# Performance work log

Measured on AMD Instinct MI355X. Metric: run time of the kernel, lower is better.

Reference implementation:

```python
import jax, jax.numpy as jnp
import numpy as np
from jax import lax

H_HID, W_HID = 8, 12
N_PAIR = H_HID * W_HID   # 96
NF = 32                  # mlp_nfilters
C_FEAT = 512 + 2         # phi_im channels + (x,y) coords


def _conv_relu(x, w, b):
    # 3x3 conv, stride 1, SAME padding (SingleConvBlock), then ReLU
    y = lax.conv_general_dilated(x, w, (1, 1), 'SAME',
                                 dimension_numbers=('NCHW', 'OIHW', 'NCHW'))
    return jax.nn.relu(y + b[None, :, None, None])


def _maxpool2(x):
    return lax.reduce_window(x, -jnp.inf, lax.max, (1, 1, 2, 2), (1, 1, 2, 2), 'VALID')


def setup_inputs() -> dict:
    key = jax.random.key(0)
    ks = jax.random.split(key, 16)
    d = {}
    d['x'] = jax.random.normal(ks[0], (4, 3, 64, 96), jnp.float32)
    d['sen_embed'] = jax.random.normal(ks[1], (4, 384), jnp.float32)

    def p(k, shape, fan_in):
        return (jax.random.normal(k, shape, jnp.float32) / np.float32(np.sqrt(fan_in)))

    d['enc1_w'] = p(ks[2], (64, 3, 3, 3), 3 * 9);      d['enc1_b'] = p(ks[3], (64,), 64)
    d['enc2_w'] = p(ks[4], (128, 64, 3, 3), 64 * 9);   d['enc2_b'] = p(ks[5], (128,), 128)
    d['enc3_w'] = p(ks[6], (256, 128, 3, 3), 128 * 9); d['enc3_b'] = p(ks[7], (256,), 256)
    d['enc4_w'] = p(ks[8], (512, 256, 3, 3), 256 * 9); d['enc4_b'] = p(ks[9], (512,), 512)
    d['g1_w'] = p(ks[10], (1412, 256), 1412);          d['g1_b'] = p(ks[11], (256,), 256)
    d['g2_w'] = p(ks[12], (256, 256), 256);            d['g2_b'] = p(ks[13], (256,), 256)
    d['g3_w'] = p(ks[14], (256, N_PAIR * NF), 256);    d['g3_b'] = p(ks[15], (N_PAIR * NF,), N_PAIR * NF)
    return d


def _forward(x, sen_embed, enc1_w, enc1_b, enc2_w, enc2_b, enc3_w, enc3_b,
             enc4_w, enc4_b, g1_w, g1_b, g2_w, g2_b, g3_w, g3_b):
    # ---- conv encoder ----
    e1 = _conv_relu(x, enc1_w, enc1_b)                     # [B,64,64,96]
    e2 = _conv_relu(_maxpool2(e1), enc2_w, enc2_b)         # [B,128,32,48]
    e3 = _conv_relu(_maxpool2(e2), enc3_w, enc3_b)         # [B,256,16,24]
    phi_im = _conv_relu(_maxpool2(e3), enc4_w, enc4_b)     # [B,512,8,12]
    B = phi_im.shape[0]

    # ---- coordinate grid (matches torch.meshgrid default 'ij' then reshape) ----
    xc = jnp.linspace(-1.0, 1.0, W_HID, dtype=phi_im.dtype)
    yc = jnp.linspace(-1.0, 1.0, H_HID, dtype=phi_im.dtype)
    xg, yg = jnp.meshgrid(xc, yc, indexing='ij')           # each [12,8]
    coord = jnp.stack([xg.reshape(H_HID, W_HID), yg.reshape(H_HID, W_HID)], axis=0)
    coord = jnp.broadcast_to(coord[None], (B, 2, H_HID, W_HID))

    # per-location features F: [B, n_pair, 514]
    F = jnp.concatenate([phi_im, coord], axis=1).reshape(B, C_FEAT, N_PAIR).transpose(0, 2, 1)

    # ---- all-pairs relation network ----
    # pair feature at (a,c) = concat(F[c], F[a], sen_embed); exploit linearity of first
    # Linear to avoid materializing the [B,n,n,1412] concat tensor (same math).
    A, Bm, Cm = g1_w[:C_FEAT], g1_w[C_FEAT:2 * C_FEAT], g1_w[2 * C_FEAT:]
    u = F @ A                                # i-part,  [B,n,256]
    v = F @ Bm                               # j-part,  [B,n,256]
    ws = sen_embed @ Cm + g1_b               # sentence part, [B,256]
    h1 = jax.nn.relu(u[:, None, :, :] + v[:, :, None, :] + ws[:, None, None, :])  # [B,n,n,256]
    h2 = jax.nn.relu(h1 @ g2_w + g2_b)                                           # [B,n,n,256]
    out = jax.nn.relu(h2 @ g3_w + g3_b)                                          # [B,n,n,3072]

    # sum over all n_pair^2 pairs, reshape to feature map [B,32,8,12]
    phi = out.sum(axis=(1, 2)).reshape(B, NF, H_HID, W_HID)
    return phi


def reference(x, sen_embed, enc1_w, enc1_b, enc2_w, enc2_b, enc3_w, enc3_b,
              enc4_w, enc4_b, g1_w, g1_b, g2_w, g2_b, g3_w, g3_b):
    return _forward(x, sen_embed, enc1_w, enc1_b, enc2_w, enc2_b, enc3_w, enc3_b,
                    enc4_w, enc4_b, g1_w, g1_b, g2_w, g2_b, g3_w, g3_b)
```

## Files before the change

kernel.cpp:

```cpp
#include <hip/hip_runtime.h>
#include <hip/hip_bf16.h>

using bf16 = __hip_bfloat16;
typedef __attribute__((ext_vector_type(8))) short short8;
typedef __attribute__((ext_vector_type(4))) float f32x4;

static __device__ __forceinline__ bf16 f2b(float x) { return __float2bfloat16(x); }
static __device__ __forceinline__ float b2f(bf16 x) { return __bfloat162float(x); }
static __device__ __forceinline__ short fb(float x) {
  bf16 h = __float2bfloat16(fmaxf(x, 0.f));
  return *(short*)&h;
}

static __device__ __forceinline__ void gload_lds16(const void* g, void* l) {
  auto gp = (const __attribute__((address_space(1))) unsigned int*)g;
  auto lp = (__attribute__((address_space(3))) unsigned int*)l;
  __builtin_amdgcn_global_load_lds(gp, lp, 16, 0, 0);
}

__global__ void conv1pool_kernel(const float* __restrict__ x, const float* __restrict__ w,
                                 const float* __restrict__ bias, bf16* __restrict__ out) {
  const int H = 64, W = 96, HW = H * W;
  __shared__ float wl[27 * 64];
  int tid = threadIdx.x;
  for (int idx = tid; idx < 27 * 64; idx += 256) {
    int k = idx >> 6, oc_ = idx & 63;
    wl[idx] = w[oc_ * 27 + k];
  }
  __syncthreads();
  int oc = tid & 63;
  int pp = blockIdx.x * 4 + (tid >> 6);
  int b = pp / 1536, rem = pp - b * 1536;
  int yp = rem / 48, xp = rem - yp * 48;
  int y0 = 2 * yp - 1, x0 = 2 * xp - 1;
  float win[3][4][4];
  #pragma unroll
  for (int ic = 0; ic < 3; ++ic) {
    const float* xsrc = x + ((size_t)b * 3 + ic) * HW;
    #pragma unroll
    for (int dy = 0; dy < 4; ++dy) {
      int yy = y0 + dy;
      #pragma unroll
      for (int dx = 0; dx < 4; ++dx) {
        int xx = x0 + dx;
        win[ic][dy][dx] = (yy >= 0 && yy < H && xx >= 0 && xx < W) ? xsrc[yy * W + xx] : 0.f;
      }
    }
  }
  float cmax = -1e30f;
  #pragma unroll
  for (int sy = 0; sy < 2; ++sy)
    #pragma unroll
    for (int sx = 0; sx < 2; ++sx) {
      float acc = 0.f;
      #pragma unroll
      for (int ic = 0; ic < 3; ++ic)
        #pragma unroll
        for (int ky = 0; ky < 3; ++ky)
          #pragma unroll
          for (int kx = 0; kx < 3; ++kx)
            acc += win[ic][sy + ky][sx + kx] * wl[(ic * 9 + ky * 3 + kx) * 64 + oc];
      cmax = fmaxf(cmax, acc);
    }
  out[(size_t)pp * 64 + oc] = f2b(fmaxf(cmax + bias[oc], 0.f));
}

__global__ void prep_kernel(const float* __restrict__ w2, const float* __restrict__ w3,
                            const float* __restrict__ w4, const float* __restrict__ g1w,
                            const float* __restrict__ sen, float* __restrict__ outz,
                            bf16* __restrict__ w2r, bf16* __restrict__ w3r,
                            bf16* __restrict__ w4r, bf16* __restrict__ wuv,
                            bf16* __restrict__ Fe, float* __restrict__ zb) {
  const int S1 = 73728, S2 = S1 + 294912, S3 = S2 + 1179648, S4 = S3 + 442368,
            S5 = S4 + 12288, S6 = S5 + 24576, S7 = S6 + 36864, S8 = S7 + 64;
  int i = blockIdx.x * 256 + threadIdx.x;
  if (i < S1) {
    int j = i, K = 576, IC = 64;
    int oc = j / K, r = j - oc * K, tap = r / IC, ic = r - tap * IC;
    w2r[j] = f2b(w2[((size_t)oc * IC + ic) * 9 + tap]);
  } else if (i < S2) {
    int j = i - S1, K = 1152, IC = 128;
    int oc = j / K, r = j - oc * K, tap = r / IC, ic = r - tap * IC;
    w3r[j] = f2b(w3[((size_t)oc * IC + ic) * 9 + tap]);
  } else if (i < S3) {
    int j = i - S2, K = 2304, IC = 256;
    int oc = j / K, r = j - oc * K, tap = r / IC, ic = r - tap * IC;
    w4r[j] = f2b(w4[((size_t)oc * IC + ic) * 9 + tap]);
  } else if (i < S4) {
    int j = i - S3;
    int n = j / 576, c = j - n * 576;
    float val = 0.f;
    if (n < 256)      { if (c < 514) val = g1w[(size_t)c * 256 + n]; }
    else if (n < 512) { if (c < 514) val = g1w[(size_t)(514 + c) * 256 + (n - 256)]; }
    else              { if (c < 384) val = g1w[(size_t)(1028 + c) * 256 + (n - 512)]; }
    wuv[j] = f2b(val);
  } else if (i < S5) {
    outz[i - S4] = 0.f;
  } else if (i < S6) {
    int j = i - S5;
    int r = j >> 6, cc = j & 63;
    int p = r % 96;
    float val = 0.f;
    if (cc == 0) val = -1.0f + 2.0f * (float)(p / 8) / 11.0f;
    else if (cc == 1) val = -1.0f + 2.0f * (float)(p % 8) / 7.0f;
    Fe[(size_t)r * 576 + 512 + cc] = f2b(val);
  } else if (i < S7) {
    int j = i - S6;
    int r = j / 576, c = j - r * 576;
    float val = (r < 4 && c < 384) ? sen[r * 384 + c] : 0.f;
    Fe[(size_t)(384 + r) * 576 + c] = f2b(val);
  } else if (i < S8) {
    zb[i - S7] = 0.f;
  }
}

__global__ void transpose2_kernel(const float* __restrict__ g2w, const float* __restrict__ g3w,
                                  bf16* __restrict__ w2t, bf16* __restrict__ w3t) {
  __shared__ bf16 t[32][33];
  int bid = blockIdx.x;
  const float* in;
  bf16* out;
  int R, C, c0, r0;
  if (bid < 64) { in = g2w; out = w2t; R = 256; C = 256; c0 = (bid & 7) * 32; r0 = (bid >> 3) * 32; }
  else { int b2 = bid - 64; in = g3w; out = w3t; R = 256; C = 3072; c0 = (b2 % 96) * 32; r0 = (b2 / 96) * 32; }
  int x = threadIdx.x & 31, y = threadIdx.x >> 5;
  for (int yy = y; yy < 32; yy += 8) {
    int r = r0 + yy, c = c0 + x;
    if (r < R && c < C) t[yy][x] = f2b(in[(size_t)r * C + c]);
  }
  __syncthreads();
  for (int yy = y; yy < 32; yy += 8) {
    int c = c0 + yy, r = r0 + x;
    if (r < R && c < C) out[(size_t)c * R + r] = t[x][yy];
  }
}

template <int CBITS, bool POOL>
__launch_bounds__(256)
__global__ void gemm_conv_kernel(const bf16* __restrict__ pin, const bf16* __restrict__ Wt,
                                 const float* __restrict__ bias, bf16* __restrict__ outb,
                                 const bf16* __restrict__ zbuf,
                                 int Hi, int Wi, int N, int ldout) {
  const int C = 1 << CBITS;
  const int K = 9 << CBITS;
  int m0 = blockIdx.y * 64, n0 = blockIdx.x * 64;
  __shared__ __align__(16) short A_lds[64 * 64];
  __shared__ __align__(16) short B_lds[64 * 64];
  int tid = threadIdx.x, w = tid >> 6, l = tid & 63;
  int quad = l >> 4, l16 = l & 15;
  f32x4 acc[4];
  #pragma unroll
  for (int nt = 0; nt < 4; ++nt)
    #pragma unroll
    for (int e = 0; e < 4; ++e) acc[nt][e] = 0.f;

  int lrow = l >> 3;
  int c_sw = (l & 7) ^ lrow;
  int ybase[2], xbase[2], bidx[2];
  #pragma unroll
  for (int i = 0; i < 2; ++i) {
    int row = m0 + w * 16 + i * 8 + lrow;
    if (POOL) {
      int pg = row >> 2, sub = row & 3;
      int Wh = Wi >> 1, HW2 = (Hi >> 1) * Wh;
      int b = pg / HW2, rem = pg - b * HW2;
      int py = rem / Wh, px = rem - py * Wh;
      bidx[i] = b; ybase[i] = 2 * py + (sub >> 1); xbase[i] = 2 * px + (sub & 1);
    } else {
      int HW = Hi * Wi;
      int b = row / HW, pix = row - b * HW;
      int yy = pix / Wi;
      bidx[i] = b; ybase[i] = yy; xbase[i] = pix - yy * Wi;
    }
  }
  const bf16* bg = Wt + (size_t)(n0 + w * 16 + lrow) * K + c_sw * 8;
  short* al = A_lds + ((size_t)w * 128 + l) * 8;
  short* bl = B_lds + ((size_t)w * 128 + l) * 8;

  for (int kc = 0; kc < K; kc += 64) {
    if (kc) __syncthreads();
    int colt = kc + c_sw * 8;
    int tap = colt >> CBITS, cc = colt & (C - 1);
    int ty = tap / 3, tx = tap - 3 * ty;
    #pragma unroll
    for (int i = 0; i < 2; ++i) {
      int yy = ybase[i] + ty - 1, xx = xbase[i] + tx - 1;
      const bf16* asrc = (yy >= 0 && yy < Hi && xx >= 0 && xx < Wi)
          ? pin + ((((size_t)(bidx[i] * Hi + yy)) * Wi + xx) << CBITS) + cc
          : zbuf;
      gload_lds16(asrc, al + i * 512);
      gload_lds16(bg + kc + (size_t)i * 8 * K, bl + i * 512);
    }
    __syncthreads();
    #pragma unroll
    for (int ks = 0; ks < 64; ks += 32) {
      int cb = (ks >> 3) + quad;
      int mr = w * 16 + l16;
      short8 af = *(const short8*)&A_lds[mr * 64 + ((cb ^ (mr & 7)) * 8)];
      #pragma unroll
      for (int nt = 0; nt < 4; ++nt) {
        int nr = nt * 16 + l16;
        short8 bf = *(const short8*)&B_lds[nr * 64 + ((cb ^ (nr & 7)) * 8)];
        acc[nt] = __builtin_amdgcn_mfma_f32_16x16x32_bf16(af, bf, acc[nt], 0, 0, 0);
      }
    }
  }
  if (POOL) {
    int pg = (m0 + w * 16 + quad * 4) >> 2;
    #pragma unroll
    for (int nt = 0; nt < 4; ++nt) {
      int gcol = n0 + nt * 16 + l16;
      float bv = bias[gcol];
      float m = fmaxf(fmaxf(acc[nt][0], acc[nt][1]), fmaxf(acc[nt][2], acc[nt][3]));
      outb[(size_t)pg * N + gcol] = f2b(fmaxf(m + bv, 0.f));
    }
  } else {
    #pragma unroll
    for (int nt = 0; nt < 4; ++nt) {
      int gcol = n0 + nt * 16 + l16;
      float bv = bias[gcol];
      #pragma unroll
      for (int r = 0; r < 4; ++r) {
        int grow = m0 + w * 16 + quad * 4 + r;
        outb[(size_t)grow * ldout + gcol] = f2b(fmaxf(acc[nt][r] + bv, 0.f));
      }
    }
  }
}

__launch_bounds__(256)
__global__ void gemm64_kernel(const bf16* __restrict__ A, const bf16* __restrict__ Wt,
                              float* __restrict__ outf, int K, int ldout) {
  int m0 = blockIdx.y * 64, n0 = blockIdx.x * 64;
  __shared__ __align__(16) short A_lds[64 * 64];
  __shared__ __align__(16) short B_lds[64 * 64];
  int tid = threadIdx.x, w = tid >> 6, l = tid & 63;
  int quad = l >> 4, l16 = l & 15;
  f32x4 acc[4];
  #pragma unroll
  for (int nt = 0; nt < 4; ++nt)
    #pragma unroll
    for (int e = 0; e < 4; ++e) acc[nt][e] = 0.f;

  int lrow = l >> 3;
  int c_sw = (l & 7) ^ lrow;
  const bf16* ag = A + (size_t)(m0 + w * 16 + lrow) * K + c_sw * 8;
  const bf16* bg = Wt + (size_t)(n0 + w * 16 + lrow) * K + c_sw * 8;
  short* al = A_lds + ((size_t)w * 128 + l) * 8;
  short* bl = B_lds + ((size_t)w * 128 + l) * 8;

  for (int kc = 0; kc < K; kc += 64) {
    if (kc) __syncthreads();
    #pragma unroll
    for (int i = 0; i < 2; ++i) {
      gload_lds16(ag + kc + (size_t)i * 8 * K, al + i * 512);
      gload_lds16(bg + kc + (size_t)i * 8 * K, bl + i * 512);
    }
    __syncthreads();
    #pragma unroll
    for (int ks = 0; ks < 64; ks += 32) {
      int cb = (ks >> 3) + quad;
      int mr = w * 16 + l16;
      short8 af = *(const short8*)&A_lds[mr * 64 + ((cb ^ (mr & 7)) * 8)];
      #pragma unroll
      for (int nt = 0; nt < 4; ++nt) {
        int nr = nt * 16 + l16;
        short8 bf = *(const short8*)&B_lds[nr * 64 + ((cb ^ (nr & 7)) * 8)];
        acc[nt] = __builtin_amdgcn_mfma_f32_16x16x32_bf16(af, bf, acc[nt], 0, 0, 0);
      }
    }
  }
  #pragma unroll
  for (int nt = 0; nt < 4; ++nt) {
    int gcol = n0 + nt * 16 + l16;
    #pragma unroll
    for (int r = 0; r < 4; ++r) {
      int grow = m0 + w * 16 + quad * 4 + r;
      outf[(size_t)grow * ldout + gcol] = acc[nt][r];
    }
  }
}

__launch_bounds__(256)
__global__ void gemm2_kernel(const float* __restrict__ uvws, const float* __restrict__ g1b,
                             const bf16* __restrict__ w2t, const float* __restrict__ g2b,
                             bf16* __restrict__ h2) {
  int b = blockIdx.z;
  int m0 = blockIdx.y * 128;
  int n0 = blockIdx.x * 128;
  __shared__ __align__(16) short A_lds[128 * 64];
  __shared__ __align__(16) short B_lds[128 * 64];
  __shared__ __align__(16) float wsl[256];
  int tid = threadIdx.x, w = tid >> 6, l = tid & 63;
  int quad = l >> 4, l16 = l & 15;
  int mw = (w >> 1) * 64, nw = (w & 1) * 64;
  f32x4 acc[4][4];
  #pragma unroll
  for (int i = 0; i < 4; ++i)
    #pragma unroll
    for (int j = 0; j < 4; ++j)
      #pragma unroll
      for (int e = 0; e < 4; ++e) acc[i][j][e] = 0.f;

  wsl[tid] = uvws[(size_t)(384 + b) * 768 + 512 + tid] + g1b[tid];

  int lrow = l >> 3;
  int c_sw = (l & 7) ^ lrow;
  const bf16* bg = w2t + (size_t)(n0 + w * 32 + lrow) * 256 + c_sw * 8;
  short* bl = B_lds + ((size_t)w * 256 + l) * 8;

  int row = tid >> 1, ks0 = (tid & 1) * 32;
  int m = m0 + row;
  int i_idx = m / 96, j_idx = m - i_idx * 96;
  const float* up = uvws + (size_t)(b * 96 + j_idx) * 768 + ks0;
  const float* vp = uvws + (size_t)(b * 96 + i_idx) * 768 + 256 + ks0;
  __syncthreads();

  for (int kc = 0; kc < 256; kc += 64) {
    if (kc) __syncthreads();
    #pragma unroll
    for (int i = 0; i < 4; ++i)
      gload_lds16(bg + kc + (size_t)i * 8 * 256, bl + i * 512);
    {
      const float4* u4 = (const float4*)(up + kc);
      const float4* v4 = (const float4*)(vp + kc);
      const float4* w4 = (const float4*)&wsl[kc + ks0];
      #pragma unroll
      for (int ch = 0; ch < 4; ++ch) {
        short8 pack;
        #pragma unroll
        for (int q = 0; q < 2; ++q) {
          float4 uu = u4[ch * 2 + q], vv = v4[ch * 2 + q], ww = w4[ch * 2 + q];
          pack[q * 4 + 0] = fb(uu.x + vv.x + ww.x);
          pack[q * 4 + 1] = fb(uu.y + vv.y + ww.y);
          pack[q * 4 + 2] = fb(uu.z + vv.z + ww.z);
          pack[q * 4 + 3] = fb(uu.w + vv.w + ww.w);
        }
        int lc = (ks0 >> 3) + ch;
        *(short8*)&A_lds[row * 64 + ((lc ^ (row & 7)) * 8)] = pack;
      }
    }
    __syncthreads();
    #pragma unroll
    for (int ks = 0; ks < 64; ks += 32) {
      int cb = (ks >> 3) + quad;
      short8 af[4], bfr[4];
      #pragma unroll
      for (int mt = 0; mt < 4; ++mt) {
        int mr = mw + mt * 16 + l16;
        af[mt] = *(const short8*)&A_lds[mr * 64 + ((cb ^ (mr & 7)) * 8)];
      }
      #pragma unroll
      for (int nt = 0; nt < 4; ++nt) {
        int nr = nw + nt * 16 + l16;
        bfr[nt] = *(const short8*)&B_lds[nr * 64 + ((cb ^ (nr & 7)) * 8)];
      }
      #pragma unroll
      for (int mt = 0; mt < 4; ++mt)
        #pragma unroll
        for (int nt = 0; nt < 4; ++nt)
          acc[mt][nt] = __builtin_amdgcn_mfma_f32_16x16x32_bf16(af[mt], bfr[nt], acc[mt][nt], 0, 0, 0);
    }
  }
  bf16* h2b = h2 + (size_t)b * 9216 * 256;
  #pragma unroll
  for (int nt = 0; nt < 4; ++nt) {
    int gcol = n0 + nw + nt * 16 + l16;
    float bias = g2b[gcol];
    #pragma unroll
    for (int mt = 0; mt < 4; ++mt) {
      #pragma unroll
      for (int r = 0; r < 4; ++r) {
        int grow = m0 + mw + mt * 16 + quad * 4 + r;
        h2b[(size_t)grow * 256 + gcol] = f2b(fmaxf(acc[mt][nt][r] + bias, 0.f));
      }
    }
  }
}

__launch_bounds__(256)
__global__ void gemm3_kernel(const bf16* __restrict__ h2, const bf16* __restrict__ w3t,
                             const float* __restrict__ g3b, float* __restrict__ phi) {
  int g = blockIdx.x;
  int x = g & 7, s = g >> 3;
  int grp = s / 24;
  int nIdx = s - grp * 24;
  int mb = grp * 8 + x;
  int b = mb / 72;
  int m0 = (mb - b * 72) * 128;
  int n0 = nIdx * 128;
  __shared__ __align__(16) short A_lds[128 * 64];
  __shared__ __align__(16) short B_lds[128 * 64];
  int tid = threadIdx.x, w = tid >> 6, l = tid & 63;
  int quad = l >> 4, l16 = l & 15;
  int mw = (w >> 1) * 64, nw = (w & 1) * 64;
  f32x4 acc[4][4];
  #pragma unroll
  for (int i = 0; i < 4; ++i)
    #pragma unroll
    for (int j = 0; j < 4; ++j)
      #pragma unroll
      for (int e = 0; e < 4; ++e) acc[i][j][e] = 0.f;

  const int K = 256;
  int lrow = l >> 3;
  int c_sw = (l & 7) ^ lrow;
  const bf16* ag = h2 + (size_t)(b * 9216 + m0 + w * 32 + lrow) * K + c_sw * 8;
  const bf16* bg = w3t + (size_t)(n0 + w * 32 + lrow) * K + c_sw * 8;
  short* al = A_lds + ((size_t)w * 256 + l) * 8;
  short* bl = B_lds + ((size_t)w * 256 + l) * 8;

  for (int kc = 0; kc < K; kc += 64) {
    if (kc) __syncthreads();
    #pragma unroll
    for (int i = 0; i < 4; ++i) {
      gload_lds16(ag + kc + (size_t)i * 8 * K, al + i * 512);
      gload_lds16(bg + kc + (size_t)i * 8 * K, bl + i * 512);
    }
    __syncthreads();
    #pragma unroll
    for (int ks = 0; ks < 64; ks += 32) {
      int cb = (ks >> 3) + quad;
      short8 af[4], bfr[4];
      #pragma unroll
      for (int mt = 0; mt < 4; ++mt) {
        int mr = mw + mt * 16 + l16;
        af[mt] = *(const short8*)&A_lds[mr * 64 + ((cb ^ (mr & 7)) * 8)];
      }
      #pragma unroll
      for (int nt = 0; nt < 4; ++nt) {
        int nr = nw + nt * 16 + l16;
        bfr[nt] = *(const short8*)&B_lds[nr * 64 + ((cb ^ (nr & 7)) * 8)];
      }
      #pragma unroll
      for (int mt = 0; mt < 4; ++mt)
        #pragma unroll
        for (int nt = 0; nt < 4; ++nt)
          acc[mt][nt] = __builtin_amdgcn_mfma_f32_16x16x32_bf16(af[mt], bfr[nt], acc[mt][nt], 0, 0, 0);
    }
  }
  #pragma unroll
  for (int nt = 0; nt < 4; ++nt) {
    int gcol = n0 + nw + nt * 16 + l16;
    float bias = g3b[gcol];
    float s2 = 0.f;
    #pragma unroll
    for (int mt = 0; mt < 4; ++mt)
      #pragma unroll
      for (int r = 0; r < 4; ++r)
        s2 += fmaxf(acc[mt][nt][r] + bias, 0.f);
    s2 += __shfl_xor(s2, 16, 64);
    s2 += __shfl_xor(s2, 32, 64);
    if (quad == 0) atomicAdd(&phi[b * 3072 + gcol], s2);
  }
}

extern "C" void kernel_launch(void* const* d_in, const int* in_sizes, int n_in,
                              void* d_out, int out_size, void* d_ws, size_t ws_size,
                              hipStream_t stream) {
  const float* x   = (const float*)d_in[0];
  const float* sen = (const float*)d_in[1];
  const float* w1  = (const float*)d_in[2];
  const float* b1  = (const float*)d_in[3];
  const float* w2  = (const float*)d_in[4];
  const float* b2  = (const float*)d_in[5];
  const float* w3  = (const float*)d_in[6];
  const float* b3  = (const float*)d_in[7];
  const float* w4  = (const float*)d_in[8];
  const float* b4  = (const float*)d_in[9];
  const float* g1w = (const float*)d_in[10];
  const float* g1b = (const float*)d_in[11];
  const float* g2w = (const float*)d_in[12];
  const float* g2b = (const float*)d_in[13];
  const float* g3w = (const float*)d_in[14];
  const float* g3b = (const float*)d_in[15];
  float* out = (float*)d_out;

  char* wsp = (char*)d_ws;
  size_t off = 0;
  auto alloc = [&](size_t bytes) {
    char* p = wsp + off;
    off += (bytes + 255) & ~(size_t)255;
    return (void*)p;
  };
  bf16* p1   = (bf16*)alloc((size_t)6144 * 64 * 2);
  bf16* p2   = (bf16*)alloc((size_t)1536 * 128 * 2);
  bf16* p3   = (bf16*)alloc((size_t)384 * 256 * 2);
  bf16* Fe   = (bf16*)alloc((size_t)448 * 576 * 2);
  bf16* wuv  = (bf16*)alloc((size_t)768 * 576 * 2);
  float* uvws = (float*)alloc((size_t)448 * 768 * 4);
  bf16* w2r  = (bf16*)alloc((size_t)128 * 576 * 2);
  bf16* w3r  = (bf16*)alloc((size_t)256 * 1152 * 2);
  bf16* w4r  = (bf16*)alloc((size_t)512 * 2304 * 2);
  bf16* w2t  = (bf16*)alloc((size_t)256 * 256 * 2);
  bf16* w3t  = (bf16*)alloc((size_t)3072 * 256 * 2);
  bf16* h2   = (bf16*)alloc((size_t)4 * 9216 * 256 * 2);
  float* zbuf = (float*)alloc((size_t)256);

  prep_kernel<<<dim3(8065), 256, 0, stream>>>(w2, w3, w4, g1w, sen, out, w2r, w3r, w4r, wuv, Fe, zbuf);
  transpose2_kernel<<<dim3(832), 256, 0, stream>>>(g2w, g3w, w2t, w3t);

  conv1pool_kernel<<<dim3(1536), 256, 0, stream>>>(x, w1, b1, p1);
  gemm_conv_kernel<6, true><<<dim3(2, 96), 256, 0, stream>>>(p1, w2r, b2, p2, (const bf16*)zbuf, 32, 48, 128, 128);
  gemm_conv_kernel<7, true><<<dim3(4, 24), 256, 0, stream>>>(p2, w3r, b3, p3, (const bf16*)zbuf, 16, 24, 256, 256);
  gemm_conv_kernel<8, false><<<dim3(8, 6), 256, 0, stream>>>(p3, w4r, b4, Fe, (const bf16*)zbuf, 8, 12, 512, 576);

  gemm64_kernel<<<dim3(12, 7), 256, 0, stream>>>(Fe, wuv, uvws, 576, 768);
  gemm2_kernel<<<dim3(2, 72, 4), 256, 0, stream>>>(uvws, g1b, w2t, g2b, h2);
  gemm3_kernel<<<dim3(6912), 256, 0, stream>>>(h2, w3t, g3b, out);
}
```

Before: 248.1 us.

## Fuse pair-MLP layers 2 and 3 via LDS-resident h2 and merge prep kernels

Replaces the separate gemm2 and gemm3 kernels with one head kernel. Each block computes a 64-row tile of h2 into shared memory and then loops over all 3072 output columns, reducing into phi with atomics. This removes the global h2 round trip (about 19 MB of bf16) and one launch. It also folds conv1pool, prep and the transpose into a single launch. In exchange each block now does a long serial loop over the N dimension with 64-row tiles and a heavy LDS footprint, which lowers occupancy and reuse of the w3t tiles.

```diff
diff --git a/kernel.cpp b/kernel.cpp
--- a/kernel.cpp
+++ b/kernel.cpp
@@ -18,120 +18,121 @@
   __builtin_amdgcn_global_load_lds(gp, lp, 16, 0, 0);
 }
 
-__global__ void conv1pool_kernel(const float* __restrict__ x, const float* __restrict__ w,
-                                 const float* __restrict__ bias, bf16* __restrict__ out) {
-  const int H = 64, W = 96, HW = H * W;
+__global__ void prep_all_kernel(const float* __restrict__ x, const float* __restrict__ w1,
+                                const float* __restrict__ b1, bf16* __restrict__ p1,
+                                const float* __restrict__ w2, const float* __restrict__ w3,
+                                const float* __restrict__ w4, const float* __restrict__ g1w,
+                                const float* __restrict__ sen, float* __restrict__ outz,
+                                bf16* __restrict__ w2r, bf16* __restrict__ w3r,
+                                bf16* __restrict__ w4r, bf16* __restrict__ wuv,
+                                bf16* __restrict__ Fe, float* __restrict__ zb,
+                                const float* __restrict__ g2w, const float* __restrict__ g3w,
+                                bf16* __restrict__ w2t, bf16* __restrict__ w3t) {
   __shared__ float wl[27 * 64];
+  __shared__ bf16 tt[32][33];
+  int bid = blockIdx.x;
   int tid = threadIdx.x;
-  for (int idx = tid; idx < 27 * 64; idx += 256) {
-    int k = idx >> 6, oc_ = idx & 63;
-    wl[idx] = w[oc_ * 27 + k];
-  }
-  __syncthreads();
-  int oc = tid & 63;
-  int pp = blockIdx.x * 4 + (tid >> 6);
-  int b = pp / 1536, rem = pp - b * 1536;
-  int yp = rem / 48, xp = rem - yp * 48;
-  int y0 = 2 * yp - 1, x0 = 2 * xp - 1;
-  float win[3][4][4];
-  #pragma unroll
-  for (int ic = 0; ic < 3; ++ic) {
-    const float* xsrc = x + ((size_t)b * 3 + ic) * HW;
-    #pragma unroll
-    for (int dy = 0; dy < 4; ++dy) {
-      int yy = y0 + dy;
-      #pragma unroll
-      for (int dx = 0; dx < 4; ++dx) {
-        int xx = x0 + dx;
-        win[ic][dy][dx] = (yy >= 0 && yy < H && xx >= 0 && xx < W) ? xsrc[yy * W + xx] : 0.f;
-      }
-    }
-  }
-  float cmax = -1e30f;
-  #pragma unroll
-  for (int sy = 0; sy < 2; ++sy)
-    #pragma unroll
-    for (int sx = 0; sx < 2; ++sx) {
-      float acc = 0.f;
-      #pragma unroll
-      for (int ic = 0; ic < 3; ++ic)
-        #pragma unroll
-        for (int ky = 0; ky < 3; ++ky)
+  if (bid < 1536) {
+    const int H = 64, W = 96, HW = H * W;
+    for (int idx = tid; idx < 27 * 64; idx += 256) {
+      int k = idx >> 6, oc_ = idx & 63;
+      wl[idx] = w1[oc_ * 27 + k];
+    }
+    __syncthreads();
+    int oc = tid & 63;
+    int pp = bid * 4 + (tid >> 6);
+    int b = pp / 1536, rem = pp - b * 1536;
+    int yp = rem / 48, xp = rem - yp * 48;
+    int y0 = 2 * yp - 1, x0 = 2 * xp - 1;
+    float win[3][4][4];
+    #pragma unroll
+    for (int ic = 0; ic < 3; ++ic) {
+      const float* xsrc = x + ((size_t)b * 3 + ic) * HW;
+      #pragma unroll
+      for (int dy = 0; dy < 4; ++dy) {
+        int yy = y0 + dy;
+        #pragma unroll
+        for (int dx = 0; dx < 4; ++dx) {
+          int xx = x0 + dx;
+          win[ic][dy][dx] = (yy >= 0 && yy < H && xx >= 0 && xx < W) ? xsrc[yy * W + xx] : 0.f;
+        }
+      }
+    }
+    float cmax = -1e30f;
+    #pragma unroll
+    for (int sy = 0; sy < 2; ++sy)
+      #pragma unroll
+      for (int sx = 0; sx < 2; ++sx) {
+        float acc = 0.f;
+        #pragma unroll
+        for (int ic = 0; ic < 3; ++ic)
           #pragma unroll
-          for (int kx = 0; kx < 3; ++kx)
-            acc += win[ic][sy + ky][sx + kx] * wl[(ic * 9 + ky * 3 + kx) * 64 + oc];
-      cmax = fmaxf(cmax, acc);
-    }
-  out[(size_t)pp * 64 + oc] = f2b(fmaxf(cmax + bias[oc], 0.f));
-}
-
-__global__ void prep_kernel(const float* __restrict__ w2, const float* __restrict__ w3,
-                            const float* __restrict__ w4, const float* __restrict__ g1w,
-                            const float* __restrict__ sen, float* __restrict__ outz,
-                            bf16* __restrict__ w2r, bf16* __restrict__ w3r,
-                            bf16* __restrict__ w4r, bf16* __restrict__ wuv,
-                            bf16* __restrict__ Fe, float* __restrict__ zb) {
-  const int S1 = 73728, S2 = S1 + 294912, S3 = S2 + 1179648, S4 = S3 + 442368,
-            S5 = S4 + 12288, S6 = S5 + 24576, S7 = S6 + 36864, S8 = S7 + 64;
-  int i = blockIdx.x * 256 + threadIdx.x;
-  if (i < S1) {
-    int j = i, K = 576, IC = 64;
-    int oc = j / K, r = j - oc * K, tap = r / IC, ic = r - tap * IC;
-    w2r[j] = f2b(w2[((size_t)oc * IC + ic) * 9 + tap]);
-  } else if (i < S2) {
-    int j = i - S1, K = 1152, IC = 128;
-    int oc = j / K, r = j - oc * K, tap = r / IC, ic = r - tap * IC;
-    w3r[j] = f2b(w3[((size_t)oc * IC + ic) * 9 + tap]);
-  } else if (i < S3) {
-    int j = i - S2, K = 2304, IC = 256;
-    int oc = j / K, r = j - oc * K, tap = r / IC, ic = r - tap * IC;
-    w4r[j] = f2b(w4[((size_t)oc * IC + ic) * 9 + tap]);
-  } else if (i < S4) {
-    int j = i - S3;
-    int n = j / 576, c = j - n * 576;
-    float val = 0.f;
-    if (n < 256)      { if (c < 514) val = g1w[(size_t)c * 256 + n]; }
-    else if (n < 512) { if (c < 514) val = g1w[(size_t)(514 + c) * 256 + (n - 256)]; }
-    else              { if (c < 384) val = g1w[(size_t)(1028 + c) * 256 + (n - 512)]; }
-    wuv[j] = f2b(val);
-  } else if (i < S5) {
-    outz[i - S4] = 0.f;
-  } else if (i < S6) {
-    int j = i - S5;
-    int r = j >> 6, cc = j & 63;
-    int p = r % 96;
-    float val = 0.f;
-    if (cc == 0) val = -1.0f + 2.0f * (float)(p / 8) / 11.0f;
-    else if (cc == 1) val = -1.0f + 2.0f * (float)(p % 8) / 7.0f;
-    Fe[(size_t)r * 576 + 512 + cc] = f2b(val);
-  } else if (i < S7) {
-    int j = i - S6;
-    int r = j / 576, c = j - r * 576;
-    float val = (r < 4 && c < 384) ? sen[r * 384 + c] : 0.f;
-    Fe[(size_t)(384 + r) * 576 + c] = f2b(val);
-  } else if (i < S8) {
-    zb[i - S7] = 0.f;
-  }
-}
-
-__global__ void transpose2_kernel(const float* __restrict__ g2w, const float* __restrict__ g3w,
-                                  bf16* __restrict__ w2t, bf16* __restrict__ w3t) {
-  __shared__ bf16 t[32][33];
-  int bid = blockIdx.x;
-  const float* in;
-  bf16* out;
-  int R, C, c0, r0;
-  if (bid < 64) { in = g2w; out = w2t; R = 256; C = 256; c0 = (bid & 7) * 32; r0 = (bid >> 3) * 32; }
-  else { int b2 = bid - 64; in = g3w; out = w3t; R = 256; C = 3072; c0 = (b2 % 96) * 32; r0 = (b2 / 96) * 32; }
-  int x = threadIdx.x & 31, y = threadIdx.x >> 5;
-  for (int yy = y; yy < 32; yy += 8) {
-    int r = r0 + yy, c = c0 + x;
-    if (r < R && c < C) t[yy][x] = f2b(in[(size_t)r * C + c]);
-  }
-  __syncthreads();
-  for (int yy = y; yy < 32; yy += 8) {
-    int c = c0 + yy, r = r0 + x;
-    if (r < R && c < C) out[(size_t)c * R + r] = t[x][yy];
+          for (int ky = 0; ky < 3; ++ky)
+            #pragma unroll
+            for (int kx = 0; kx < 3; ++kx)
+              acc += win[ic][sy + ky][sx + kx] * wl[(ic * 9 + ky * 3 + kx) * 64 + oc];
+        cmax = fmaxf(cmax, acc);
+      }
+    p1[(size_t)pp * 64 + oc] = f2b(fmaxf(cmax + b1[oc], 0.f));
+  } else if (bid < 9601) {
+    const int S1 = 73728, S2 = S1 + 294912, S3 = S2 + 1179648, S4 = S3 + 442368,
+              S5 = S4 + 12288, S6 = S5 + 24576, S7 = S6 + 36864, S8 = S7 + 64;
+    int i = (bid - 1536) * 256 + tid;
+    if (i < S1) {
+      int j = i, K = 576, IC = 64;
+      int oc = j / K, r = j - oc * K, tap = r / IC, ic = r - tap * IC;
+      w2r[j] = f2b(w2[((size_t)oc * IC + ic) * 9 + tap]);
+    } else if (i < S2) {
+      int j = i - S1, K = 1152, IC = 128;
+      int oc = j / K, r = j - oc * K, tap = r / IC, ic = r - tap * IC;
+      w3r[j] = f2b(w3[((size_t)oc * IC + ic) * 9 + tap]);
+    } else if (i < S3) {
+      int j = i - S2, K = 2304, IC = 256;
+      int oc = j / K, r = j - oc * K, tap = r / IC, ic = r - tap * IC;
+      w4r[j] = f2b(w4[((size_t)oc * IC + ic) * 9 + tap]);
+    } else if (i < S4) {
+      int j = i - S3;
+      int n = j / 576, c = j - n * 576;
+      float val = 0.f;
+      if (n < 256)      { if (c < 514) val = g1w[(size_t)c * 256 + n]; }
+      else if (n < 512) { if (c < 514) val = g1w[(size_t)(514 + c) * 256 + (n - 256)]; }
+      else              { if (c < 384) val = g1w[(size_t)(1028 + c) * 256 + (n - 512)]; }
+      wuv[j] = f2b(val);
+    } else if (i < S5) {
+      outz[i - S4] = 0.f;
+    } else if (i < S6) {
+      int j = i - S5;
+      int r = j >> 6, cc = j & 63;
+      int p = r % 96;
+      float val = 0.f;
+      if (cc == 0) val = -1.0f + 2.0f * (float)(p / 8) / 11.0f;
+      else if (cc == 1) val = -1.0f + 2.0f * (float)(p % 8) / 7.0f;
+      Fe[(size_t)r * 576 + 512 + cc] = f2b(val);
+    } else if (i < S7) {
+      int j = i - S6;
+      int r = j / 576, c = j - r * 576;
+      float val = (r < 4 && c < 384) ? sen[r * 384 + c] : 0.f;
+      Fe[(size_t)(384 + r) * 576 + c] = f2b(val);
+    } else if (i < S8) {
+      zb[i - S7] = 0.f;
+    }
+  } else {
+    int b2 = bid - 9601;
+    const float* in;
+    bf16* out;
+    int R = 256, C, c0, r0;
+    if (b2 < 64) { in = g2w; out = w2t; C = 256; c0 = (b2 & 7) * 32; r0 = (b2 >> 3) * 32; }
+    else { b2 -= 64; in = g3w; out = w3t; C = 3072; c0 = (b2 % 96) * 32; r0 = (b2 / 96) * 32; }
+    int xq = tid & 31, yq = tid >> 5;
+    for (int yy = yq; yy < 32; yy += 8) {
+      int r = r0 + yy, c = c0 + xq;
+      if (r < R && c < C) tt[yy][xq] = f2b(in[(size_t)r * C + c]);
+    }
+    __syncthreads();
+    for (int yy = yq; yy < 32; yy += 8) {
+      int c = c0 + yy, r = r0 + xq;
+      if (r < R && c < C) out[(size_t)c * R + r] = tt[xq][yy];
+    }
   }
 }
 
@@ -200,8 +201,8 @@
       #pragma unroll
       for (int nt = 0; nt < 4; ++nt) {
         int nr = nt * 16 + l16;
-        short8 bf = *(const short8*)&B_lds[nr * 64 + ((cb ^ (nr & 7)) * 8)];
-        acc[nt] = __builtin_amdgcn_mfma_f32_16x16x32_bf16(af, bf, acc[nt], 0, 0, 0);
+        short8 bf2 = *(const short8*)&B_lds[nr * 64 + ((cb ^ (nr & 7)) * 8)];
+        acc[nt] = __builtin_amdgcn_mfma_f32_16x16x32_bf16(af, bf2, acc[nt], 0, 0, 0);
       }
     }
   }
@@ -265,8 +266,8 @@
       #pragma unroll
       for (int nt = 0; nt < 4; ++nt) {
         int nr = nt * 16 + l16;
-        short8 bf = *(const short8*)&B_lds[nr * 64 + ((cb ^ (nr & 7)) * 8)];
-        acc[nt] = __builtin_amdgcn_mfma_f32_16x16x32_bf16(af, bf, acc[nt], 0, 0, 0);
+        short8 bf2 = *(const short8*)&B_lds[nr * 64 + ((cb ^ (nr & 7)) * 8)];
+        acc[nt] = __builtin_amdgcn_mfma_f32_16x16x32_bf16(af, bf2, acc[nt], 0, 0, 0);
       }
     }
   }
@@ -282,18 +283,28 @@
 }
 
 __launch_bounds__(256)
-__global__ void gemm2_kernel(const float* __restrict__ uvws, const float* __restrict__ g1b,
-                             const bf16* __restrict__ w2t, const float* __restrict__ g2b,
-                             bf16* __restrict__ h2) {
-  int b = blockIdx.z;
-  int m0 = blockIdx.y * 128;
-  int n0 = blockIdx.x * 128;
-  __shared__ __align__(16) short A_lds[128 * 64];
-  __shared__ __align__(16) short B_lds[128 * 64];
-  __shared__ __align__(16) float wsl[256];
+__global__ void head_kernel(const float* __restrict__ uvws, const float* __restrict__ g1b,
+                            const bf16* __restrict__ w2t, const float* __restrict__ g2b,
+                            const bf16* __restrict__ w3t, const float* __restrict__ g3b,
+                            float* __restrict__ out) {
+  __shared__ __align__(16) short h2l[64 * 256];
+  __shared__ __align__(16) short Breg[10240];
+  __shared__ float g3bl[3072];
+  __shared__ float g2bl[256];
+  __shared__ float wsl[256];
+  int blk = blockIdx.x;
+  int b = blk / 144;
+  int m0g = (blk - b * 144) * 64;
   int tid = threadIdx.x, w = tid >> 6, l = tid & 63;
   int quad = l >> 4, l16 = l & 15;
-  int mw = (w >> 1) * 64, nw = (w & 1) * 64;
+
+  wsl[tid] = uvws[(size_t)(384 + b) * 768 + 512 + tid] + g1b[tid];
+  g2bl[tid] = g2b[tid];
+  #pragma unroll
+  for (int i = 0; i < 12; ++i) g3bl[i * 256 + tid] = g3b[i * 256 + tid];
+
+  short* A2 = Breg;
+  short* B2 = Breg + 2048;
   f32x4 acc[4][4];
   #pragma unroll
   for (int i = 0; i < 4; ++i)
@@ -302,156 +313,128 @@
       #pragma unroll
       for (int e = 0; e < 4; ++e) acc[i][j][e] = 0.f;
 
-  wsl[tid] = uvws[(size_t)(384 + b) * 768 + 512 + tid] + g1b[tid];
-
-  int lrow = l >> 3;
-  int c_sw = (l & 7) ^ lrow;
-  const bf16* bg = w2t + (size_t)(n0 + w * 32 + lrow) * 256 + c_sw * 8;
-  short* bl = B_lds + ((size_t)w * 256 + l) * 8;
-
-  int row = tid >> 1, ks0 = (tid & 1) * 32;
-  int m = m0 + row;
-  int i_idx = m / 96, j_idx = m - i_idx * 96;
-  const float* up = uvws + (size_t)(b * 96 + j_idx) * 768 + ks0;
-  const float* vp = uvws + (size_t)(b * 96 + i_idx) * 768 + 256 + ks0;
+  int arow = tid >> 2, aseg = tid & 3;
+  int mA = m0g + arow;
+  int i_idx = mA / 96, j_idx = mA - i_idx * 96;
+  const float* up = uvws + (size_t)(b * 96 + j_idx) * 768;
+  const float* vp = uvws + (size_t)(b * 96 + i_idx) * 768 + 256;
+  int brow = w * 64 + ((l >> 2) << 4) + 0;
   __syncthreads();
 
-  for (int kc = 0; kc < 256; kc += 64) {
-    if (kc) __syncthreads();
+  for (int kc2 = 0; kc2 < 8; ++kc2) {
+    if (kc2) __syncthreads();
+    {
+      int k0 = kc2 * 32 + aseg * 8;
+      float4 ua = *(const float4*)(up + k0), ub = *(const float4*)(up + k0 + 4);
+      float4 va = *(const float4*)(vp + k0), vb = *(const float4*)(vp + k0 + 4);
+      float4 wa = *(const float4*)&wsl[k0], wb = *(const float4*)&wsl[k0 + 4];
+      short8 pack;
+      pack[0] = fb(ua.x + va.x + wa.x); pack[1] = fb(ua.y + va.y + wa.y);
+      pack[2] = fb(ua.z + va.z + wa.z); pack[3] = fb(ua.w + va.w + wa.w);
+      pack[4] = fb(ub.x + vb.x + wb.x); pack[5] = fb(ub.y + vb.y + wb.y);
+      pack[6] = fb(ub.z + vb.z + wb.z); pack[7] = fb(ub.w + vb.w + wb.w);
+      *(short8*)&A2[arow * 32 + ((aseg ^ (arow & 3)) * 8)] = pack;
+    }
+    {
+      #pragma unroll
+      for (int i = 0; i < 4; ++i) {
+        int r16 = w * 64 + i * 16 + (l >> 2);
+        int cq = (l & 3) ^ (r16 & 3);
+        gload_lds16(w2t + (size_t)r16 * 256 + kc2 * 32 + cq * 8, B2 + w * 2048 + i * 512 + l * 8);
+      }
+    }
+    __syncthreads();
+    short8 af[4], bfr[4];
+    #pragma unroll
+    for (int mt = 0; mt < 4; ++mt) {
+      int mr = mt * 16 + l16;
+      af[mt] = *(const short8*)&A2[mr * 32 + ((quad ^ (mr & 3)) * 8)];
+    }
+    #pragma unroll
+    for (int nt = 0; nt < 4; ++nt) {
+      int nr = w * 64 + nt * 16 + l16;
+      bfr[nt] = *(const short8*)&B2[nr * 32 + ((quad ^ (nr & 3)) * 8)];
+    }
+    #pragma unroll
+    for (int mt = 0; mt < 4; ++mt)
+      #pragma unroll
+      for (int nt = 0; nt < 4; ++nt)
+        acc[mt][nt] = __builtin_amdgcn_mfma_f32_16x16x32_bf16(af[mt], bfr[nt], acc[mt][nt], 0, 0, 0);
+  }
+  #pragma unroll
+  for (int nt = 0; nt < 4; ++nt) {
+    int gcol = w * 64 + nt * 16 + l16;
+    float bv = g2bl[gcol];
+    #pragma unroll
+    for (int mt = 0; mt < 4; ++mt) {
+      #pragma unroll
+      for (int r = 0; r < 4; ++r) {
+        int grow = mt * 16 + quad * 4 + r;
+        h2l[grow * 256 + (((gcol >> 3) ^ (grow & 7)) * 8) + (gcol & 7)] =
+            fb(acc[mt][nt][r] + bv);
+      }
+    }
+  }
+  __syncthreads();
+
+  short* B3 = Breg;
+  for (int nt24 = 0; nt24 < 24; ++nt24) {
+    f32x4 acc3[4][2];
     #pragma unroll
     for (int i = 0; i < 4; ++i)
-      gload_lds16(bg + kc + (size_t)i * 8 * 256, bl + i * 512);
-    {
-      const float4* u4 = (const float4*)(up + kc);
-      const float4* v4 = (const float4*)(vp + kc);
-      const float4* w4 = (const float4*)&wsl[kc + ks0];
-      #pragma unroll
-      for (int ch = 0; ch < 4; ++ch) {
-        short8 pack;
-        #pragma unroll
-        for (int q = 0; q < 2; ++q) {
-          float4 uu = u4[ch * 2 + q], vv = v4[ch * 2 + q], ww = w4[ch * 2 + q];
-          pack[q * 4 + 0] = fb(uu.x + vv.x + ww.x);
-          pack[q * 4 + 1] = fb(uu.y + vv.y + ww.y);
-          pack[q * 4 + 2] = fb(uu.z + vv.z + ww.z);
-          pack[q * 4 + 3] = fb(uu.w + vv.w + ww.w);
+      #pragma unroll
+      for (int j = 0; j < 2; ++j)
+        #pragma unroll
+        for (int e = 0; e < 4; ++e) acc3[i][j][e] = 0.f;
+    for (int kc = 0; kc < 4; ++kc) {
+      __syncthreads();
+      {
+        int lrow = l >> 3;
+        int c_sw = (l & 7) ^ lrow;
+        #pragma unroll
+        for (int i = 0; i < 4; ++i) {
+          int nrow = nt24 * 128 + w * 32 + i * 8 + lrow;
+          gload_lds16(w3t + (size_t)nrow * 256 + kc * 64 + c_sw * 8,
+                      B3 + w * 2048 + i * 512 + l * 8);
         }
-        int lc = (ks0 >> 3) + ch;
-        *(short8*)&A_lds[row * 64 + ((lc ^ (row & 7)) * 8)] = pack;
-      }
-    }
-    __syncthreads();
-    #pragma unroll
-    for (int ks = 0; ks < 64; ks += 32) {
-      int cb = (ks >> 3) + quad;
-      short8 af[4], bfr[4];
-      #pragma unroll
-      for (int mt = 0; mt < 4; ++mt) {
-        int mr = mw + mt * 16 + l16;
-        af[mt] = *(const short8*)&A_lds[mr * 64 + ((cb ^ (mr & 7)) * 8)];
-      }
-      #pragma unroll
-      for (int nt = 0; nt < 4; ++nt) {
-        int nr = nw + nt * 16 + l16;
-        bfr[nt] = *(const short8*)&B_lds[nr * 64 + ((cb ^ (nr & 7)) * 8)];
-      }
+      }
+      __syncthreads();
+      #pragma unroll
+      for (int ks = 0; ks < 64; ks += 32) {
+        short8 af[4], bfr[2];
+        #pragma unroll
+        for (int mt = 0; mt < 4; ++mt) {
+          int mr = mt * 16 + l16;
+          int Cc = kc * 8 + (ks >> 3) + quad;
+          af[mt] = *(const short8*)&h2l[mr * 256 + ((Cc ^ (mr & 7)) * 8)];
+        }
+        #pragma unroll
+        for (int nt = 0; nt < 2; ++nt) {
+          int nr = w * 32 + nt * 16 + l16;
+          int cb = (ks >> 3) + quad;
+          bfr[nt] = *(const short8*)&B3[nr * 64 + ((cb ^ (nr & 7)) * 8)];
+        }
+        #pragma unroll
+        for (int mt = 0; mt < 4; ++mt)
+          #pragma unroll
+          for (int nt = 0; nt < 2; ++nt)
+            acc3[mt][nt] = __builtin_amdgcn_mfma_f32_16x16x32_bf16(af[mt], bfr[nt], acc3[mt][nt], 0, 0, 0);
+      }
+    }
+    #pragma unroll
+    for (int nt = 0; nt < 2; ++nt) {
+      int gcol = nt24 * 128 + w * 32 + nt * 16 + l16;
+      float bias = g3bl[gcol];
+      float s2 = 0.f;
       #pragma unroll
       for (int mt = 0; mt < 4; ++mt)
         #pragma unroll
-        for (int nt = 0; nt < 4; ++nt)
-          acc[mt][nt] = __builtin_amdgcn_mfma_f32_16x16x32_bf16(af[mt], bfr[nt], acc[mt][nt], 0, 0, 0);
-    }
-  }
-  bf16* h2b = h2 + (size_t)b * 9216 * 256;
-  #pragma unroll
-  for (int nt = 0; nt < 4; ++nt) {
-    int gcol = n0 + nw + nt * 16 + l16;
-    float bias = g2b[gcol];
-    #pragma unroll
-    for (int mt = 0; mt < 4; ++mt) {
-      #pragma unroll
-      for (int r = 0; r < 4; ++r) {
-        int grow = m0 + mw + mt * 16 + quad * 4 + r;
-        h2b[(size_t)grow * 256 + gcol] = f2b(fmaxf(acc[mt][nt][r] + bias, 0.f));
-      }
-    }
-  }
-}
-
-__launch_bounds__(256)
-__global__ void gemm3_kernel(const bf16* __restrict__ h2, const bf16* __restrict__ w3t,
-                             const float* __restrict__ g3b, float* __restrict__ phi) {
-  int g = blockIdx.x;
-  int x = g & 7, s = g >> 3;
-  int grp = s / 24;
-  int nIdx = s - grp * 24;
-  int mb = grp * 8 + x;
-  int b = mb / 72;
-  int m0 = (mb - b * 72) * 128;
-  int n0 = nIdx * 128;
-  __shared__ __align__(16) short A_lds[128 * 64];
-  __shared__ __align__(16) short B_lds[128 * 64];
-  int tid = threadIdx.x, w = tid >> 6, l = tid & 63;
-  int quad = l >> 4, l16 = l & 15;
-  int mw = (w >> 1) * 64, nw = (w & 1) * 64;
-  f32x4 acc[4][4];
-  #pragma unroll
-  for (int i = 0; i < 4; ++i)
-    #pragma unroll
-    for (int j = 0; j < 4; ++j)
-      #pragma unroll
-      for (int e = 0; e < 4; ++e) acc[i][j][e] = 0.f;
-
-  const int K = 256;
-  int lrow = l >> 3;
-  int c_sw = (l & 7) ^ lrow;
-  const bf16* ag = h2 + (size_t)(b * 9216 + m0 + w * 32 + lrow) * K + c_sw * 8;
-  const bf16* bg = w3t + (size_t)(n0 + w * 32 + lrow) * K + c_sw * 8;
-  short* al = A_lds + ((size_t)w * 256 + l) * 8;
-  short* bl = B_lds + ((size_t)w * 256 + l) * 8;
-
-  for (int kc = 0; kc < K; kc += 64) {
-    if (kc) __syncthreads();
-    #pragma unroll
-    for (int i = 0; i < 4; ++i) {
-      gload_lds16(ag + kc + (size_t)i * 8 * K, al + i * 512);
-      gload_lds16(bg + kc + (size_t)i * 8 * K, bl + i * 512);
-    }
-    __syncthreads();
-    #pragma unroll
-    for (int ks = 0; ks < 64; ks += 32) {
-      int cb = (ks >> 3) + quad;
-      short8 af[4], bfr[4];
-      #pragma unroll
-      for (int mt = 0; mt < 4; ++mt) {
-        int mr = mw + mt * 16 + l16;
-        af[mt] = *(const short8*)&A_lds[mr * 64 + ((cb ^ (mr & 7)) * 8)];
-      }
-      #pragma unroll
-      for (int nt = 0; nt < 4; ++nt) {
-        int nr = nw + nt * 16 + l16;
-        bfr[nt] = *(const short8*)&B_lds[nr * 64 + ((cb ^ (nr & 7)) * 8)];
-      }
-      #pragma unroll
-      for (int mt = 0; mt < 4; ++mt)
-        #pragma unroll
-        for (int nt = 0; nt < 4; ++nt)
-          acc[mt][nt] = __builtin_amdgcn_mfma_f32_16x16x32_bf16(af[mt], bfr[nt], acc[mt][nt], 0, 0, 0);
-    }
-  }
-  #pragma unroll
-  for (int nt = 0; nt < 4; ++nt) {
-    int gcol = n0 + nw + nt * 16 + l16;
-    float bias = g3b[gcol];
-    float s2 = 0.f;
-    #pragma unroll
-    for (int mt = 0; mt < 4; ++mt)
-      #pragma unroll
-      for (int r = 0; r < 4; ++r)
-        s2 += fmaxf(acc[mt][nt][r] + bias, 0.f);
-    s2 += __shfl_xor(s2, 16, 64);
-    s2 += __shfl_xor(s2, 32, 64);
-    if (quad == 0) atomicAdd(&phi[b * 3072 + gcol], s2);
+        for (int r = 0; r < 4; ++r)
+          s2 += fmaxf(acc3[mt][nt][r] + bias, 0.f);
+      s2 += __shfl_xor(s2, 16, 64);
+      s2 += __shfl_xor(s2, 32, 64);
+      if (quad == 0) atomicAdd(&out[b * 3072 + gcol], s2);
+    }
   }
 }
 
@@ -494,18 +477,15 @@
   bf16* w4r  = (bf16*)alloc((size_t)512 * 2304 * 2);
   bf16* w2t  = (bf16*)alloc((size_t)256 * 256 * 2);
   bf16* w3t  = (bf16*)alloc((size_t)3072 * 256 * 2);
-  bf16* h2   = (bf16*)alloc((size_t)4 * 9216 * 256 * 2);
   float* zbuf = (float*)alloc((size_t)256);
 
-  prep_kernel<<<dim3(8065), 256, 0, stream>>>(w2, w3, w4, g1w, sen, out, w2r, w3r, w4r, wuv, Fe, zbuf);
-  transpose2_kernel<<<dim3(832), 256, 0, stream>>>(g2w, g3w, w2t, w3t);
-
-  conv1pool_kernel<<<dim3(1536), 256, 0, stream>>>(x, w1, b1, p1);
+  prep_all_kernel<<<dim3(10433), 256, 0, stream>>>(x, w1, b1, p1, w2, w3, w4, g1w, sen, out,
+                                                   w2r, w3r, w4r, wuv, Fe, zbuf, g2w, g3w, w2t, w3t);
+
   gemm_conv_kernel<6, true><<<dim3(2, 96), 256, 0, stream>>>(p1, w2r, b2, p2, (const bf16*)zbuf, 32, 48, 128, 128);
   gemm_conv_kernel<7, true><<<dim3(4, 24), 256, 0, stream>>>(p2, w3r, b3, p3, (const bf16*)zbuf, 16, 24, 256, 256);
   gemm_conv_kernel<8, false><<<dim3(8, 6), 256, 0, stream>>>(p3, w4r, b4, Fe, (const bf16*)zbuf, 8, 12, 512, 576);
 
   gemm64_kernel<<<dim3(12, 7), 256, 0, stream>>>(Fe, wuv, uvws, 576, 768);
-  gemm2_kernel<<<dim3(2, 72, 4), 256, 0, stream>>>(uvws, g1b, w2t, g2b, h2);
-  gemm3_kernel<<<dim3(6912), 256, 0, stream>>>(h2, w3t, g3b, out);
-}
+  head_kernel<<<dim3(576), 256, 0, stream>>>(uvws, g1b, w2t, g2b, w3t, g3b, out);
+}
```

Result: slower. 325.8 us (+31.3%).
